# Kernel tuning notes

Hardware: AMD Instinct MI355X
Metric: run time of the kernel (lower is better)

Reference implementation:

```python
import jax, jax.numpy as jnp
import numpy as np

B, T, E, H = 2, 2048, 2048, 16
D = E // H  # head dim = 128
ROPE_BASE = 10000.0


def setup_inputs() -> dict:
    key = jax.random.key(0)
    ks = jax.random.split(key, 9)
    s = 1.0 / np.sqrt(E)
    return {
        "x": jax.random.normal(ks[0], (B, T, E), jnp.float32),
        "Wq": jax.random.normal(ks[1], (E, E), jnp.float32) * s,
        "bq": jax.random.normal(ks[2], (E,), jnp.float32) * s,
        "Wk": jax.random.normal(ks[3], (E, E), jnp.float32) * s,
        "bk": jax.random.normal(ks[4], (E,), jnp.float32) * s,
        "Wv": jax.random.normal(ks[5], (E, E), jnp.float32) * s,
        "bv": jax.random.normal(ks[6], (E,), jnp.float32) * s,
        "Wo": jax.random.normal(ks[7], (E, E), jnp.float32) * s,
        "bo": jax.random.normal(ks[8], (E,), jnp.float32) * s,
    }


def _rope(x):
    # x: [b, h, t, d]; positions are 1-indexed (m+1) as in the source
    t, d = x.shape[-2], x.shape[-1]
    j = jnp.arange(d // 2, dtype=x.dtype)
    thetas = ROPE_BASE ** (-2.0 * j / d)                  # [d/2]
    m = jnp.arange(1, t + 1, dtype=x.dtype)               # [t]
    ang = m[:, None] * thetas[None, :]                    # [t, d/2]
    C = jnp.concatenate([ang, ang], axis=-1)              # [t, d]
    x_rot = jnp.concatenate([-x[..., d // 2:], x[..., :d // 2]], axis=-1)
    return x * jnp.cos(C) + x_rot * jnp.sin(C)


def reference(x, Wq, bq, Wk, bk, Wv, bv, Wo, bo):
    b, t, e = x.shape
    # projections (nn.Linear: x @ W.T + b)
    def proj(W, bias):
        y = jnp.einsum('bte,fe->btf', x, W) + bias
        return y.reshape(b, t, H, D).transpose(0, 2, 1, 3)  # b h t d
    q = _rope(proj(Wq, bq))
    k = _rope(proj(Wk, bk))
    v = proj(Wv, bv)

    scale = jnp.sqrt(jnp.asarray(D, x.dtype))
    att = jnp.einsum('bhqd,bhkd->bhqk', q, k) / scale
    causal = jnp.tril(jnp.ones((t, t), bool))
    att = jnp.where(causal, att, -jnp.inf)
    att = jax.nn.softmax(att, axis=-1)
    y = jnp.einsum('bhqk,bhkd->bhqd', att, v)
    y = y.transpose(0, 2, 1, 3).reshape(b, t, e)
    y = jnp.einsum('bte,fe->btf', y, Wo) + bo
    return y
```

## Files before the change

kernel.cpp:

```cpp
#include <hip/hip_runtime.h>
#include <hip/hip_bf16.h>

typedef __bf16 bf16_t;
typedef __bf16 bf16x4 __attribute__((ext_vector_type(4)));
typedef __bf16 bf16x8 __attribute__((ext_vector_type(8)));
typedef float  f32x4  __attribute__((ext_vector_type(4)));

#define GLD_LDS16(gptr, lptr)                                                        \
    __builtin_amdgcn_global_load_lds((__attribute__((address_space(1))) void*)(gptr),\
                                     (__attribute__((address_space(3))) void*)(lptr),\
                                     16, 0, 0)

constexpr int Bc = 2, Tc = 2048, Ec = 2048, Hc = 16, Dc = 128;
constexpr int Mtok = Bc * Tc;

__device__ __forceinline__ bf16x8 cvt8(const float* p) {
    f32x4 a = *(const f32x4*)p;
    f32x4 b = *(const f32x4*)(p + 4);
    bf16x8 r;
    r[0] = (bf16_t)a[0]; r[1] = (bf16_t)a[1];
    r[2] = (bf16_t)a[2]; r[3] = (bf16_t)a[3];
    r[4] = (bf16_t)b[0]; r[5] = (bf16_t)b[1];
    r[6] = (bf16_t)b[2]; r[7] = (bf16_t)b[3];
    return r;
}

__global__ void convert_bf16(const float* __restrict__ src, bf16_t* __restrict__ dst) {
    size_t i = ((size_t)blockIdx.x * 256 + threadIdx.x) * 8;
    *(bf16x8*)&dst[i] = cvt8(src + i);
}

__global__ void convert_w(const float* __restrict__ Wq, const float* __restrict__ Wk,
                          const float* __restrict__ Wv, const float* __restrict__ Wo,
                          bf16_t* __restrict__ w4) {
    int blk = blockIdx.x;
    int wi  = blk >> 11;
    const float* src = (wi == 0) ? Wq : (wi == 1) ? Wk : (wi == 2) ? Wv : Wo;
    bf16_t* dst = w4 + (size_t)wi * Ec * Ec;
    size_t i = ((size_t)(blk & 2047) * 256 + threadIdx.x) * 8;
    *(bf16x8*)&dst[i] = cvt8(src + i);
}

__global__ __launch_bounds__(256) void gemm_qkv_bf(const bf16_t* __restrict__ A,
                                                   const bf16_t* __restrict__ w3,
                                                   const float* __restrict__ bq,
                                                   const float* __restrict__ bk,
                                                   const float* __restrict__ bv,
                                                   bf16_t* __restrict__ qo,
                                                   bf16_t* __restrict__ ko,
                                                   bf16_t* __restrict__ vto) {
    __shared__ __align__(16) bf16_t ldsA[128 * 32];
    __shared__ __align__(16) bf16_t ldsB[128 * 32];

    const int tid  = threadIdx.x;
    const int wave = tid >> 6;
    const int lane = tid & 63;
    const int g    = lane >> 4;
    const int n16  = lane & 15;
    const int m0   = blockIdx.x * 128;
    const int mat  = blockIdx.y >> 4;
    const int n0   = (blockIdx.y & 15) * 128;
    const int row_off = (wave >> 1) * 64;
    const int col_off = (wave & 1) * 64;
    const int K = Ec;

    const bf16_t* W   = w3 + (size_t)mat * Ec * Ec;
    const float* bias = (mat == 0) ? bq : (mat == 1) ? bk : bv;

    f32x4 acc[4][4] = {};

    const int r0 = tid >> 2;
    const int cc = tid & 3;
    const size_t a0 = (size_t)(m0 + r0) * K + cc * 8;
    const size_t a1 = (size_t)(m0 + r0 + 64) * K + cc * 8;
    const size_t b0 = (size_t)(n0 + r0) * K + cc * 8;
    const size_t b1 = (size_t)(n0 + r0 + 64) * K + cc * 8;

    for (int k0 = 0; k0 < K; k0 += 32) {
        __syncthreads();
        GLD_LDS16(A + a0 + k0, &ldsA[(wave * 64) * 8]);
        GLD_LDS16(A + a1 + k0, &ldsA[(256 + wave * 64) * 8]);
        GLD_LDS16(W + b0 + k0, &ldsB[(wave * 64) * 8]);
        GLD_LDS16(W + b1 + k0, &ldsB[(256 + wave * 64) * 8]);
        __syncthreads();

        bf16x8 af[4], bfr[4];
#pragma unroll
        for (int mt = 0; mt < 4; ++mt)
            af[mt] = *(const bf16x8*)&ldsA[(row_off + mt * 16 + n16) * 32 + g * 8];
#pragma unroll
        for (int nt = 0; nt < 4; ++nt)
            bfr[nt] = *(const bf16x8*)&ldsB[(col_off + nt * 16 + n16) * 32 + g * 8];
#pragma unroll
        for (int mt = 0; mt < 4; ++mt)
#pragma unroll
            for (int nt = 0; nt < 4; ++nt)
                acc[mt][nt] = __builtin_amdgcn_mfma_f32_16x16x32_bf16(
                    af[mt], bfr[nt], acc[mt][nt], 0, 0, 0);
    }

#pragma unroll
    for (int nt = 0; nt < 4; ++nt) {
        int n = n0 + col_off + nt * 16 + n16;
        float bn = bias[n];
        int h = n >> 7, d = n & (Dc - 1);
#pragma unroll
        for (int mt = 0; mt < 4; ++mt) {
            int mb = m0 + row_off + mt * 16 + g * 4;
            int b = mb >> 11, t = mb & (Tc - 1);
            if (mat == 2) {
                bf16x4 pk;
#pragma unroll
                for (int r = 0; r < 4; ++r) pk[r] = (bf16_t)(acc[mt][nt][r] + bn);
                *(bf16x4*)&vto[(((size_t)(b * Hc + h)) * Dc + d) * Tc + t] = pk;
            } else {
                bf16_t* outb = (mat == 0) ? qo : ko;
#pragma unroll
                for (int r = 0; r < 4; ++r)
                    outb[(((size_t)(b * Hc + h)) * Tc + (t + r)) * Dc + d] =
                        (bf16_t)(acc[mt][nt][r] + bn);
            }
        }
    }
}

__global__ __launch_bounds__(256) void gemm_out_bf(const bf16_t* __restrict__ A,
                                                   const bf16_t* __restrict__ W,
                                                   const float* __restrict__ bias,
                                                   float* __restrict__ out,
                                                   int M, int N, int K) {
    __shared__ __align__(16) bf16_t ldsA[128 * 32];
    __shared__ __align__(16) bf16_t ldsB[128 * 32];

    const int tid  = threadIdx.x;
    const int wave = tid >> 6;
    const int lane = tid & 63;
    const int g    = lane >> 4;
    const int n16  = lane & 15;
    const int m0 = blockIdx.x * 128;
    const int n0 = blockIdx.y * 128;
    const int row_off = (wave >> 1) * 64;
    const int col_off = (wave & 1) * 64;

    f32x4 acc[4][4] = {};

    const int r0 = tid >> 2;
    const int cc = tid & 3;
    const size_t a0 = (size_t)(m0 + r0) * K + cc * 8;
    const size_t a1 = (size_t)(m0 + r0 + 64) * K + cc * 8;
    const size_t b0 = (size_t)(n0 + r0) * K + cc * 8;
    const size_t b1 = (size_t)(n0 + r0 + 64) * K + cc * 8;

    for (int k0 = 0; k0 < K; k0 += 32) {
        __syncthreads();
        GLD_LDS16(A + a0 + k0, &ldsA[(wave * 64) * 8]);
        GLD_LDS16(A + a1 + k0, &ldsA[(256 + wave * 64) * 8]);
        GLD_LDS16(W + b0 + k0, &ldsB[(wave * 64) * 8]);
        GLD_LDS16(W + b1 + k0, &ldsB[(256 + wave * 64) * 8]);
        __syncthreads();

        bf16x8 af[4], bfr[4];
#pragma unroll
        for (int mt = 0; mt < 4; ++mt)
            af[mt] = *(const bf16x8*)&ldsA[(row_off + mt * 16 + n16) * 32 + g * 8];
#pragma unroll
        for (int nt = 0; nt < 4; ++nt)
            bfr[nt] = *(const bf16x8*)&ldsB[(col_off + nt * 16 + n16) * 32 + g * 8];
#pragma unroll
        for (int mt = 0; mt < 4; ++mt)
#pragma unroll
            for (int nt = 0; nt < 4; ++nt)
                acc[mt][nt] = __builtin_amdgcn_mfma_f32_16x16x32_bf16(
                    af[mt], bfr[nt], acc[mt][nt], 0, 0, 0);
    }

#pragma unroll
    for (int nt = 0; nt < 4; ++nt) {
        int n = n0 + col_off + nt * 16 + n16;
        float bn = bias[n];
#pragma unroll
        for (int mt = 0; mt < 4; ++mt) {
            int mb = m0 + row_off + mt * 16 + g * 4;
#pragma unroll
            for (int r = 0; r < 4; ++r)
                out[(size_t)(mb + r) * N + n] = acc[mt][nt][r] + bn;
        }
    }
}

__global__ __launch_bounds__(256) void gemm_qkv(const bf16_t* __restrict__ A,
                                                const float* __restrict__ Wq,
                                                const float* __restrict__ Wk,
                                                const float* __restrict__ Wv,
                                                const float* __restrict__ bq,
                                                const float* __restrict__ bk,
                                                const float* __restrict__ bv,
                                                bf16_t* __restrict__ qo,
                                                bf16_t* __restrict__ ko,
                                                bf16_t* __restrict__ vto) {
    __shared__ __align__(16) bf16_t ldsA[128 * 32];
    __shared__ __align__(16) bf16_t ldsB[128 * 32];

    const int tid  = threadIdx.x;
    const int wave = tid >> 6;
    const int lane = tid & 63;
    const int g    = lane >> 4;
    const int n16  = lane & 15;
    const int m0   = blockIdx.x * 128;
    const int mat  = blockIdx.y >> 4;
    const int n0   = (blockIdx.y & 15) * 128;
    const int row_off = (wave >> 1) * 64;
    const int col_off = (wave & 1) * 64;
    const int K = Ec;

    const float* W    = (mat == 0) ? Wq : (mat == 1) ? Wk : Wv;
    const float* bias = (mat == 0) ? bq : (mat == 1) ? bk : bv;

    f32x4 acc[4][4] = {};

    const int r0 = tid >> 2;
    const int cc = tid & 3;
    const size_t a0 = (size_t)(m0 + r0) * K + cc * 8;
    const size_t a1 = (size_t)(m0 + r0 + 64) * K + cc * 8;
    const float* pb0 = W + (size_t)(n0 + r0) * K + cc * 8;
    const float* pb1 = W + (size_t)(n0 + r0 + 64) * K + cc * 8;

    for (int k0 = 0; k0 < K; k0 += 32) {
        bf16x8 vb0 = cvt8(pb0 + k0);
        bf16x8 vb1 = cvt8(pb1 + k0);
        __syncthreads();
        GLD_LDS16(A + a0 + k0, &ldsA[(wave * 64) * 8]);
        GLD_LDS16(A + a1 + k0, &ldsA[(256 + wave * 64) * 8]);
        *(bf16x8*)&ldsB[(size_t)tid * 8]         = vb0;
        *(bf16x8*)&ldsB[(size_t)(256 + tid) * 8] = vb1;
        __syncthreads();

        bf16x8 af[4], bfr[4];
#pragma unroll
        for (int mt = 0; mt < 4; ++mt)
            af[mt] = *(const bf16x8*)&ldsA[(row_off + mt * 16 + n16) * 32 + g * 8];
#pragma unroll
        for (int nt = 0; nt < 4; ++nt)
            bfr[nt] = *(const bf16x8*)&ldsB[(col_off + nt * 16 + n16) * 32 + g * 8];
#pragma unroll
        for (int mt = 0; mt < 4; ++mt)
#pragma unroll
            for (int nt = 0; nt < 4; ++nt)
                acc[mt][nt] = __builtin_amdgcn_mfma_f32_16x16x32_bf16(
                    af[mt], bfr[nt], acc[mt][nt], 0, 0, 0);
    }

#pragma unroll
    for (int nt = 0; nt < 4; ++nt) {
        int n = n0 + col_off + nt * 16 + n16;
        float bn = bias[n];
        int h = n >> 7, d = n & (Dc - 1);
#pragma unroll
        for (int mt = 0; mt < 4; ++mt) {
            int mb = m0 + row_off + mt * 16 + g * 4;
            int b = mb >> 11, t = mb & (Tc - 1);
            if (mat == 2) {
                bf16x4 pk;
#pragma unroll
                for (int r = 0; r < 4; ++r) pk[r] = (bf16_t)(acc[mt][nt][r] + bn);
                *(bf16x4*)&vto[(((size_t)(b * Hc + h)) * Dc + d) * Tc + t] = pk;
            } else {
                bf16_t* outb = (mat == 0) ? qo : ko;
#pragma unroll
                for (int r = 0; r < 4; ++r)
                    outb[(((size_t)(b * Hc + h)) * Tc + (t + r)) * Dc + d] =
                        (bf16_t)(acc[mt][nt][r] + bn);
            }
        }
    }
}

__global__ __launch_bounds__(256) void gemm_out(const bf16_t* __restrict__ A,
                                                const float* __restrict__ W,
                                                const float* __restrict__ bias,
                                                float* __restrict__ out,
                                                int M, int N, int K) {
    __shared__ __align__(16) bf16_t ldsA[128 * 32];
    __shared__ __align__(16) bf16_t ldsB[128 * 32];

    const int tid  = threadIdx.x;
    const int wave = tid >> 6;
    const int lane = tid & 63;
    const int g    = lane >> 4;
    const int n16  = lane & 15;
    const int m0 = blockIdx.x * 128;
    const int n0 = blockIdx.y * 128;
    const int row_off = (wave >> 1) * 64;
    const int col_off = (wave & 1) * 64;

    f32x4 acc[4][4] = {};

    const int r0 = tid >> 2;
    const int cc = tid & 3;
    const size_t a0 = (size_t)(m0 + r0) * K + cc * 8;
    const size_t a1 = (size_t)(m0 + r0 + 64) * K + cc * 8;
    const float* pb0 = W + (size_t)(n0 + r0) * K + cc * 8;
    const float* pb1 = W + (size_t)(n0 + r0 + 64) * K + cc * 8;

    for (int k0 = 0; k0 < K; k0 += 32) {
        bf16x8 vb0 = cvt8(pb0 + k0);
        bf16x8 vb1 = cvt8(pb1 + k0);
        __syncthreads();
        GLD_LDS16(A + a0 + k0, &ldsA[(wave * 64) * 8]);
        GLD_LDS16(A + a1 + k0, &ldsA[(256 + wave * 64) * 8]);
        *(bf16x8*)&ldsB[(size_t)tid * 8]         = vb0;
        *(bf16x8*)&ldsB[(size_t)(256 + tid) * 8] = vb1;
        __syncthreads();

        bf16x8 af[4], bfr[4];
#pragma unroll
        for (int mt = 0; mt < 4; ++mt)
            af[mt] = *(const bf16x8*)&ldsA[(row_off + mt * 16 + n16) * 32 + g * 8];
#pragma unroll
        for (int nt = 0; nt < 4; ++nt)
            bfr[nt] = *(const bf16x8*)&ldsB[(col_off + nt * 16 + n16) * 32 + g * 8];
#pragma unroll
        for (int mt = 0; mt < 4; ++mt)
#pragma unroll
            for (int nt = 0; nt < 4; ++nt)
                acc[mt][nt] = __builtin_amdgcn_mfma_f32_16x16x32_bf16(
                    af[mt], bfr[nt], acc[mt][nt], 0, 0, 0);
    }

#pragma unroll
    for (int nt = 0; nt < 4; ++nt) {
        int n = n0 + col_off + nt * 16 + n16;
        float bn = bias[n];
#pragma unroll
        for (int mt = 0; mt < 4; ++mt) {
            int mb = m0 + row_off + mt * 16 + g * 4;
#pragma unroll
            for (int r = 0; r < 4; ++r)
                out[(size_t)(mb + r) * N + n] = acc[mt][nt][r] + bn;
        }
    }
}

__global__ void rope_kernel(bf16_t* __restrict__ q, bf16_t* __restrict__ k) {
    int row = blockIdx.x * 4 + (threadIdx.x >> 6);
    int d   = threadIdx.x & 63;
    int t   = row & (Tc - 1);
    float theta = powf(10000.0f, -(float)d * (1.0f / 64.0f));
    float ang   = (float)(t + 1) * theta;
    float sv, cv;
    sincosf(ang, &sv, &cv);
    size_t base = (size_t)row * Dc;
    float q1 = (float)q[base + d], q2 = (float)q[base + d + 64];
    q[base + d]      = (bf16_t)(q1 * cv - q2 * sv);
    q[base + d + 64] = (bf16_t)(q2 * cv + q1 * sv);
    float k1 = (float)k[base + d], k2 = (float)k[base + d + 64];
    k[base + d]      = (bf16_t)(k1 * cv - k2 * sv);
    k[base + d + 64] = (bf16_t)(k2 * cv + k1 * sv);
}

constexpr int KP = 128 + 8;
constexpr int VP = 64 + 8;
constexpr int PP = 64 + 8;

__global__ __launch_bounds__(256) void attn_kernel(const bf16_t* __restrict__ q,
                                                   const bf16_t* __restrict__ kmat,
                                                   const bf16_t* __restrict__ vt,
                                                   bf16_t* __restrict__ out) {
    __shared__ __align__(16) bf16_t k_lds[64 * KP];
    __shared__ __align__(16) bf16_t v_lds[128 * VP];
    __shared__ __align__(16) bf16_t p_lds[4 * 16 * PP];

    const int tid  = threadIdx.x;
    const int wave = tid >> 6, lane = tid & 63;
    const int g = lane >> 4, n16 = lane & 15;
    const int pi = blockIdx.x;
    const int bh = blockIdx.y;
    const size_t base = (size_t)bh * Tc * Dc;
    const int b = bh >> 4, h = bh & 15;
    const float sc2 = 0.08838834764831845f * 1.4426950408889634f;
    bf16_t* pw = &p_lds[wave * 16 * PP];

    const int kr_key = tid >> 4, kr_c = tid & 15;
    const int vr_dd  = tid >> 3, vr_c = tid & 7;

#pragma unroll 1
    for (int half = 0; half < 2; ++half) {
        const int qt = half ? pi : 31 - pi;
        const int q0 = qt * 64;

        bf16x8 qf[4];
        {
            const bf16_t* qp = q + base + (size_t)(q0 + wave * 16 + n16) * Dc + g * 8;
#pragma unroll
            for (int kk = 0; kk < 4; ++kk) qf[kk] = *(const bf16x8*)(qp + kk * 32);
        }

        float m_run[4], l_run[4];
#pragma unroll
        for (int r = 0; r < 4; ++r) { m_run[r] = -1e30f; l_run[r] = 0.0f; }
        f32x4 o_acc[8] = {};

        bf16x8 rk[4], rv[4];
#pragma unroll
        for (int i = 0; i < 4; ++i)
            rk[i] = *(const bf16x8*)&kmat[base + (size_t)(i * 16 + kr_key) * Dc + kr_c * 8];
#pragma unroll
        for (int i = 0; i < 4; ++i)
            rv[i] = *(const bf16x8*)&vt[base + (size_t)(i * 32 + vr_dd) * Tc + vr_c * 8];

#pragma unroll 1
        for (int kt = 0; kt <= qt; ++kt) {
            const int k0 = kt * 64;
            __syncthreads();
#pragma unroll
            for (int i = 0; i < 4; ++i)
                *(bf16x8*)&k_lds[(i * 16 + kr_key) * KP + kr_c * 8] = rk[i];
#pragma unroll
            for (int i = 0; i < 4; ++i)
                *(bf16x8*)&v_lds[(i * 32 + vr_dd) * VP + vr_c * 8] = rv[i];
            __syncthreads();

            if (kt < qt) {
                const int kn = k0 + 64;
#pragma unroll
                for (int i = 0; i < 4; ++i)
                    rk[i] = *(const bf16x8*)&kmat[base + (size_t)(kn + i * 16 + kr_key) * Dc + kr_c * 8];
#pragma unroll
                for (int i = 0; i < 4; ++i)
                    rv[i] = *(const bf16x8*)&vt[base + (size_t)(i * 32 + vr_dd) * Tc + kn + vr_c * 8];
            }

            f32x4 s_acc[4];
#pragma unroll
            for (int nt = 0; nt < 4; ++nt) {
                f32x4 a = {};
                int key = nt * 16 + n16;
#pragma unroll
                for (int kk = 0; kk < 4; ++kk) {
                    bf16x8 kf = *(const bf16x8*)&k_lds[key * KP + kk * 32 + g * 8];
                    a = __builtin_amdgcn_mfma_f32_16x16x32_bf16(qf[kk], kf, a, 0, 0, 0);
                }
                s_acc[nt] = a;
            }

            if (kt == qt) {
#pragma unroll
                for (int nt = 0; nt < 4; ++nt) {
                    int key = k0 + nt * 16 + n16;
#pragma unroll
                    for (int r = 0; r < 4; ++r) {
                        int qq = q0 + wave * 16 + g * 4 + r;
                        float v = s_acc[nt][r] * sc2;
                        s_acc[nt][r] = (key <= qq) ? v : -1e30f;
                    }
                }
            } else {
#pragma unroll
                for (int nt = 0; nt < 4; ++nt)
#pragma unroll
                    for (int r = 0; r < 4; ++r) s_acc[nt][r] *= sc2;
            }

            float alpha[4];
#pragma unroll
            for (int r = 0; r < 4; ++r) {
                float rm = fmaxf(fmaxf(s_acc[0][r], s_acc[1][r]),
                                 fmaxf(s_acc[2][r], s_acc[3][r]));
                rm = fmaxf(rm, __shfl_xor(rm, 1, 16));
                rm = fmaxf(rm, __shfl_xor(rm, 2, 16));
                rm = fmaxf(rm, __shfl_xor(rm, 4, 16));
                rm = fmaxf(rm, __shfl_xor(rm, 8, 16));
                float m_new = fmaxf(m_run[r], rm);
                alpha[r] = __builtin_amdgcn_exp2f(m_run[r] - m_new);
                m_run[r] = m_new;
                float sum = 0.0f;
#pragma unroll
                for (int nt = 0; nt < 4; ++nt) {
                    float p = __builtin_amdgcn_exp2f(s_acc[nt][r] - m_new);
                    s_acc[nt][r] = p;
                    sum += p;
                }
                l_run[r] = l_run[r] * alpha[r] + sum;
            }
#pragma unroll
            for (int dt = 0; dt < 8; ++dt)
#pragma unroll
                for (int r = 0; r < 4; ++r) o_acc[dt][r] *= alpha[r];

#pragma unroll
            for (int nt = 0; nt < 4; ++nt) {
                int key = nt * 16 + n16;
#pragma unroll
                for (int r = 0; r < 4; ++r)
                    pw[(g * 4 + r) * PP + key] = (bf16_t)s_acc[nt][r];
            }
            bf16x8 pf[2];
#pragma unroll
            for (int kk = 0; kk < 2; ++kk)
                pf[kk] = *(const bf16x8*)&pw[n16 * PP + kk * 32 + g * 8];

#pragma unroll
            for (int dt = 0; dt < 8; ++dt) {
                int dd = dt * 16 + n16;
#pragma unroll
                for (int kk = 0; kk < 2; ++kk) {
                    bf16x8 vf = *(const bf16x8*)&v_lds[dd * VP + kk * 32 + g * 8];
                    o_acc[dt] = __builtin_amdgcn_mfma_f32_16x16x32_bf16(
                        pf[kk], vf, o_acc[dt], 0, 0, 0);
                }
            }
        }

        float inv_l[4];
#pragma unroll
        for (int r = 0; r < 4; ++r) {
            float s = l_run[r];
            s += __shfl_xor(s, 1, 16);
            s += __shfl_xor(s, 2, 16);
            s += __shfl_xor(s, 4, 16);
            s += __shfl_xor(s, 8, 16);
            inv_l[r] = 1.0f / s;
        }
#pragma unroll
        for (int dt = 0; dt < 8; ++dt) {
            int d = dt * 16 + n16;
#pragma unroll
            for (int r = 0; r < 4; ++r) {
                int qq = q0 + wave * 16 + g * 4 + r;
                out[((size_t)(b * Tc + qq)) * Ec + h * Dc + d] =
                    (bf16_t)(o_acc[dt][r] * inv_l[r]);
            }
        }
    }
}

extern "C" void kernel_launch(void* const* d_in, const int* in_sizes, int n_in,
                              void* d_out, int out_size, void* d_ws, size_t ws_size,
                              hipStream_t stream) {
    const float* x  = (const float*)d_in[0];
    const float* Wq = (const float*)d_in[1];
    const float* bq = (const float*)d_in[2];
    const float* Wk = (const float*)d_in[3];
    const float* bk = (const float*)d_in[4];
    const float* Wv = (const float*)d_in[5];
    const float* bv = (const float*)d_in[6];
    const float* Wo = (const float*)d_in[7];
    const float* bo = (const float*)d_in[8];
    float* out = (float*)d_out;

    char* ws = (char*)d_ws;
    const size_t sz  = (size_t)Bc * Hc * Tc * Dc * sizeof(bf16_t);
    const size_t szW = (size_t)Ec * Ec * sizeof(bf16_t);
    bf16_t* q   = (bf16_t*)(ws);
    bf16_t* k   = (bf16_t*)(ws + sz);
    bf16_t* vt  = (bf16_t*)(ws + 2 * sz);
    bf16_t* xb  = (bf16_t*)(ws + 3 * sz);
    bf16_t* att = xb;

    if (ws_size >= 4 * sz + 4 * szW) {
        bf16_t* w4 = (bf16_t*)(ws + 4 * sz);
        convert_bf16<<<Mtok * Ec / (256 * 8), 256, 0, stream>>>(x, xb);
        convert_w<<<8192, 256, 0, stream>>>(Wq, Wk, Wv, Wo, w4);
        gemm_qkv_bf<<<dim3(Mtok / 128, 48), 256, 0, stream>>>(xb, w4, bq, bk, bv,
                                                              q, k, vt);
        rope_kernel<<<Bc * Hc * Tc / 4, 256, 0, stream>>>(q, k);
        attn_kernel<<<dim3(16, Bc * Hc), 256, 0, stream>>>(q, k, vt, att);
        gemm_out_bf<<<dim3(Mtok / 128, Ec / 128), 256, 0, stream>>>(
            att, w4 + 3 * (size_t)Ec * Ec, bo, out, Mtok, Ec, Ec);
    } else {
        convert_bf16<<<Mtok * Ec / (256 * 8), 256, 0, stream>>>(x, xb);
        gemm_qkv<<<dim3(Mtok / 128, 48), 256, 0, stream>>>(xb, Wq, Wk, Wv,
                                                           bq, bk, bv, q, k, vt);
        rope_kernel<<<Bc * Hc * Tc / 4, 256, 0, stream>>>(q, k);
        attn_kernel<<<dim3(16, Bc * Hc), 256, 0, stream>>>(q, k, vt, att);
        gemm_out<<<dim3(Mtok / 128, Ec / 128), 256, 0, stream>>>(att, Wo, bo, out,
                                                                 Mtok, Ec, Ec);
    }
}
```

Before: 434.1 us.

## Triple-buffer bf16 projection GEMMs with 256x128 tiles and swizzled LDS

Replaces the QKV and output projection GEMMs with 512-thread, 256x128-tile kernels that keep three LDS stages and prefetch two K-steps ahead using direct global-to-LDS loads. They wait on vmcnt instead of double __syncthreads and XOR-swizzle the LDS columns to avoid bank conflicts. MFMA sections are raised in priority. This targets the load-to-compute stalls of the single-buffered loop, at the cost of more LDS per block and hand-counted waitcnt logic that could break if the load count changes.

```diff
diff --git a/kernel.cpp b/kernel.cpp
--- a/kernel.cpp
+++ b/kernel.cpp
@@ -41,64 +41,94 @@
     *(bf16x8*)&dst[i] = cvt8(src + i);
 }
 
-__global__ __launch_bounds__(256) void gemm_qkv_bf(const bf16_t* __restrict__ A,
-                                                   const bf16_t* __restrict__ w3,
-                                                   const float* __restrict__ bq,
-                                                   const float* __restrict__ bk,
-                                                   const float* __restrict__ bv,
-                                                   bf16_t* __restrict__ qo,
-                                                   bf16_t* __restrict__ ko,
-                                                   bf16_t* __restrict__ vto) {
-    __shared__ __align__(16) bf16_t ldsA[128 * 32];
-    __shared__ __align__(16) bf16_t ldsB[128 * 32];
+
+__global__ __launch_bounds__(512, 2) void gemm_qkv_p(const bf16_t* __restrict__ A,
+                                                     const bf16_t* __restrict__ w3,
+                                                     const float* __restrict__ bq,
+                                                     const float* __restrict__ bk,
+                                                     const float* __restrict__ bv,
+                                                     bf16_t* __restrict__ qo,
+                                                     bf16_t* __restrict__ ko,
+                                                     bf16_t* __restrict__ vto) {
+    __shared__ __align__(16) bf16_t ldsA[3 * 256 * 32];
+    __shared__ __align__(16) bf16_t ldsB[3 * 128 * 32];
 
     const int tid  = threadIdx.x;
     const int wave = tid >> 6;
     const int lane = tid & 63;
     const int g    = lane >> 4;
     const int n16  = lane & 15;
-    const int m0   = blockIdx.x * 128;
+    const int wm   = wave >> 1;
+    const int wn   = wave & 1;
+    const int m0   = blockIdx.x * 256;
     const int mat  = blockIdx.y >> 4;
     const int n0   = (blockIdx.y & 15) * 128;
-    const int row_off = (wave >> 1) * 64;
-    const int col_off = (wave & 1) * 64;
-    const int K = Ec;
+    const int K    = Ec;
 
     const bf16_t* W   = w3 + (size_t)mat * Ec * Ec;
     const float* bias = (mat == 0) ? bq : (mat == 1) ? bk : bv;
 
+    const int sr   = tid >> 2;
+    const int scol = (((tid & 3) ^ ((tid >> 3) & 3)) << 3);
+    const bf16_t* gA0 = A + (size_t)(m0 + sr) * K + scol;
+    const bf16_t* gA1 = A + (size_t)(m0 + 128 + sr) * K + scol;
+    const bf16_t* gB  = W + (size_t)(n0 + sr) * K + scol;
+    const int dL = wave * 512;
+
+    const int fsw = (n16 >> 1) & 3;
+    const int rAo = (wm * 64 + n16) * 32 + ((g ^ fsw) << 3);
+    const int rBo = (wn * 64 + n16) * 32 + ((g ^ fsw) << 3);
+
     f32x4 acc[4][4] = {};
 
-    const int r0 = tid >> 2;
-    const int cc = tid & 3;
-    const size_t a0 = (size_t)(m0 + r0) * K + cc * 8;
-    const size_t a1 = (size_t)(m0 + r0 + 64) * K + cc * 8;
-    const size_t b0 = (size_t)(n0 + r0) * K + cc * 8;
-    const size_t b1 = (size_t)(n0 + r0 + 64) * K + cc * 8;
-
-    for (int k0 = 0; k0 < K; k0 += 32) {
-        __syncthreads();
-        GLD_LDS16(A + a0 + k0, &ldsA[(wave * 64) * 8]);
-        GLD_LDS16(A + a1 + k0, &ldsA[(256 + wave * 64) * 8]);
-        GLD_LDS16(W + b0 + k0, &ldsB[(wave * 64) * 8]);
-        GLD_LDS16(W + b1 + k0, &ldsB[(256 + wave * 64) * 8]);
-        __syncthreads();
-
+    constexpr int NT = Ec / 32;
+#pragma unroll
+    for (int tt = 0; tt < 2; ++tt) {
+        GLD_LDS16(gA0 + tt * 32, &ldsA[tt * 8192 + dL]);
+        GLD_LDS16(gA1 + tt * 32, &ldsA[tt * 8192 + 4096 + dL]);
+        GLD_LDS16(gB  + tt * 32, &ldsB[tt * 4096 + dL]);
+    }
+
+    int bc = 0;
+    int bi = 2;
+#pragma unroll 1
+    for (int t = 0; t < NT; ++t) {
+        if (t < NT - 1) { asm volatile("s_waitcnt vmcnt(3)" ::: "memory"); }
+        else            { asm volatile("s_waitcnt vmcnt(0)" ::: "memory"); }
+        __builtin_amdgcn_s_barrier();
+        asm volatile("" ::: "memory");
+
+        const bf16_t* la = &ldsA[bc * 8192];
+        const bf16_t* lb = &ldsB[bc * 4096];
         bf16x8 af[4], bfr[4];
 #pragma unroll
-        for (int mt = 0; mt < 4; ++mt)
-            af[mt] = *(const bf16x8*)&ldsA[(row_off + mt * 16 + n16) * 32 + g * 8];
-#pragma unroll
-        for (int nt = 0; nt < 4; ++nt)
-            bfr[nt] = *(const bf16x8*)&ldsB[(col_off + nt * 16 + n16) * 32 + g * 8];
+        for (int mt = 0; mt < 4; ++mt) af[mt] = *(const bf16x8*)&la[rAo + mt * 512];
+#pragma unroll
+        for (int nt = 0; nt < 4; ++nt) bfr[nt] = *(const bf16x8*)&lb[rBo + nt * 512];
+
+        if (t + 2 < NT) {
+            GLD_LDS16(gA0 + (t + 2) * 32, &ldsA[bi * 8192 + dL]);
+            GLD_LDS16(gA1 + (t + 2) * 32, &ldsA[bi * 8192 + 4096 + dL]);
+            GLD_LDS16(gB  + (t + 2) * 32, &ldsB[bi * 4096 + dL]);
+        }
+
+        asm volatile("s_waitcnt lgkmcnt(0)" ::: "memory");
+        __builtin_amdgcn_sched_barrier(0);
+        __builtin_amdgcn_s_setprio(1);
 #pragma unroll
         for (int mt = 0; mt < 4; ++mt)
 #pragma unroll
             for (int nt = 0; nt < 4; ++nt)
                 acc[mt][nt] = __builtin_amdgcn_mfma_f32_16x16x32_bf16(
                     af[mt], bfr[nt], acc[mt][nt], 0, 0, 0);
-    }
-
+        __builtin_amdgcn_s_setprio(0);
+
+        bc = (bc == 2) ? 0 : bc + 1;
+        bi = (bi == 2) ? 0 : bi + 1;
+    }
+
+    const int row_off = wm * 64;
+    const int col_off = wn * 64;
 #pragma unroll
     for (int nt = 0; nt < 4; ++nt) {
         int n = n0 + col_off + nt * 16 + n16;
@@ -107,73 +137,101 @@
 #pragma unroll
         for (int mt = 0; mt < 4; ++mt) {
             int mb = m0 + row_off + mt * 16 + g * 4;
-            int b = mb >> 11, t = mb & (Tc - 1);
+            int b = mb >> 11, tk = mb & (Tc - 1);
             if (mat == 2) {
                 bf16x4 pk;
 #pragma unroll
                 for (int r = 0; r < 4; ++r) pk[r] = (bf16_t)(acc[mt][nt][r] + bn);
-                *(bf16x4*)&vto[(((size_t)(b * Hc + h)) * Dc + d) * Tc + t] = pk;
+                *(bf16x4*)&vto[(((size_t)(b * Hc + h)) * Dc + d) * Tc + tk] = pk;
             } else {
                 bf16_t* outb = (mat == 0) ? qo : ko;
 #pragma unroll
                 for (int r = 0; r < 4; ++r)
-                    outb[(((size_t)(b * Hc + h)) * Tc + (t + r)) * Dc + d] =
+                    outb[(((size_t)(b * Hc + h)) * Tc + (tk + r)) * Dc + d] =
                         (bf16_t)(acc[mt][nt][r] + bn);
             }
         }
     }
 }
 
-__global__ __launch_bounds__(256) void gemm_out_bf(const bf16_t* __restrict__ A,
-                                                   const bf16_t* __restrict__ W,
-                                                   const float* __restrict__ bias,
-                                                   float* __restrict__ out,
-                                                   int M, int N, int K) {
-    __shared__ __align__(16) bf16_t ldsA[128 * 32];
-    __shared__ __align__(16) bf16_t ldsB[128 * 32];
+__global__ __launch_bounds__(512, 2) void gemm_out_p(const bf16_t* __restrict__ A,
+                                                     const bf16_t* __restrict__ W,
+                                                     const float* __restrict__ bias,
+                                                     float* __restrict__ out) {
+    __shared__ __align__(16) bf16_t ldsA[3 * 256 * 32];
+    __shared__ __align__(16) bf16_t ldsB[3 * 128 * 32];
 
     const int tid  = threadIdx.x;
     const int wave = tid >> 6;
     const int lane = tid & 63;
     const int g    = lane >> 4;
     const int n16  = lane & 15;
-    const int m0 = blockIdx.x * 128;
-    const int n0 = blockIdx.y * 128;
-    const int row_off = (wave >> 1) * 64;
-    const int col_off = (wave & 1) * 64;
+    const int wm   = wave >> 1;
+    const int wn   = wave & 1;
+    const int m0   = blockIdx.x * 256;
+    const int n0   = blockIdx.y * 128;
+    const int K    = Ec;
+
+    const int sr   = tid >> 2;
+    const int scol = (((tid & 3) ^ ((tid >> 3) & 3)) << 3);
+    const bf16_t* gA0 = A + (size_t)(m0 + sr) * K + scol;
+    const bf16_t* gA1 = A + (size_t)(m0 + 128 + sr) * K + scol;
+    const bf16_t* gB  = W + (size_t)(n0 + sr) * K + scol;
+    const int dL = wave * 512;
+
+    const int fsw = (n16 >> 1) & 3;
+    const int rAo = (wm * 64 + n16) * 32 + ((g ^ fsw) << 3);
+    const int rBo = (wn * 64 + n16) * 32 + ((g ^ fsw) << 3);
 
     f32x4 acc[4][4] = {};
 
-    const int r0 = tid >> 2;
-    const int cc = tid & 3;
-    const size_t a0 = (size_t)(m0 + r0) * K + cc * 8;
-    const size_t a1 = (size_t)(m0 + r0 + 64) * K + cc * 8;
-    const size_t b0 = (size_t)(n0 + r0) * K + cc * 8;
-    const size_t b1 = (size_t)(n0 + r0 + 64) * K + cc * 8;
-
-    for (int k0 = 0; k0 < K; k0 += 32) {
-        __syncthreads();
-        GLD_LDS16(A + a0 + k0, &ldsA[(wave * 64) * 8]);
-        GLD_LDS16(A + a1 + k0, &ldsA[(256 + wave * 64) * 8]);
-        GLD_LDS16(W + b0 + k0, &ldsB[(wave * 64) * 8]);
-        GLD_LDS16(W + b1 + k0, &ldsB[(256 + wave * 64) * 8]);
-        __syncthreads();
-
+    constexpr int NT = Ec / 32;
+#pragma unroll
+    for (int tt = 0; tt < 2; ++tt) {
+        GLD_LDS16(gA0 + tt * 32, &ldsA[tt * 8192 + dL]);
+        GLD_LDS16(gA1 + tt * 32, &ldsA[tt * 8192 + 4096 + dL]);
+        GLD_LDS16(gB  + tt * 32, &ldsB[tt * 4096 + dL]);
+    }
+
+    int bc = 0, bi = 2;
+#pragma unroll 1
+    for (int t = 0; t < NT; ++t) {
+        if (t < NT - 1) { asm volatile("s_waitcnt vmcnt(3)" ::: "memory"); }
+        else            { asm volatile("s_waitcnt vmcnt(0)" ::: "memory"); }
+        __builtin_amdgcn_s_barrier();
+        asm volatile("" ::: "memory");
+
+        const bf16_t* la = &ldsA[bc * 8192];
+        const bf16_t* lb = &ldsB[bc * 4096];
         bf16x8 af[4], bfr[4];
 #pragma unroll
-        for (int mt = 0; mt < 4; ++mt)
-            af[mt] = *(const bf16x8*)&ldsA[(row_off + mt * 16 + n16) * 32 + g * 8];
-#pragma unroll
-        for (int nt = 0; nt < 4; ++nt)
-            bfr[nt] = *(const bf16x8*)&ldsB[(col_off + nt * 16 + n16) * 32 + g * 8];
+        for (int mt = 0; mt < 4; ++mt) af[mt] = *(const bf16x8*)&la[rAo + mt * 512];
+#pragma unroll
+        for (int nt = 0; nt < 4; ++nt) bfr[nt] = *(const bf16x8*)&lb[rBo + nt * 512];
+
+        if (t + 2 < NT) {
+            GLD_LDS16(gA0 + (t + 2) * 32, &ldsA[bi * 8192 + dL]);
+            GLD_LDS16(gA1 + (t + 2) * 32, &ldsA[bi * 8192 + 4096 + dL]);
+            GLD_LDS16(gB  + (t + 2) * 32, &ldsB[bi * 4096 + dL]);
+        }
+
+        asm volatile("s_waitcnt lgkmcnt(0)" ::: "memory");
+        __builtin_amdgcn_sched_barrier(0);
+        __builtin_amdgcn_s_setprio(1);
 #pragma unroll
         for (int mt = 0; mt < 4; ++mt)
 #pragma unroll
             for (int nt = 0; nt < 4; ++nt)
                 acc[mt][nt] = __builtin_amdgcn_mfma_f32_16x16x32_bf16(
                     af[mt], bfr[nt], acc[mt][nt], 0, 0, 0);
-    }
-
+        __builtin_amdgcn_s_setprio(0);
+
+        bc = (bc == 2) ? 0 : bc + 1;
+        bi = (bi == 2) ? 0 : bi + 1;
+    }
+
+    const int row_off = wm * 64;
+    const int col_off = wn * 64;
 #pragma unroll
     for (int nt = 0; nt < 4; ++nt) {
         int n = n0 + col_off + nt * 16 + n16;
@@ -183,7 +241,7 @@
             int mb = m0 + row_off + mt * 16 + g * 4;
 #pragma unroll
             for (int r = 0; r < 4; ++r)
-                out[(size_t)(mb + r) * N + n] = acc[mt][nt][r] + bn;
+                out[(size_t)(mb + r) * Ec + n] = acc[mt][nt][r] + bn;
         }
     }
 }
@@ -561,12 +619,12 @@
         bf16_t* w4 = (bf16_t*)(ws + 4 * sz);
         convert_bf16<<<Mtok * Ec / (256 * 8), 256, 0, stream>>>(x, xb);
         convert_w<<<8192, 256, 0, stream>>>(Wq, Wk, Wv, Wo, w4);
-        gemm_qkv_bf<<<dim3(Mtok / 128, 48), 256, 0, stream>>>(xb, w4, bq, bk, bv,
-                                                              q, k, vt);
+        gemm_qkv_p<<<dim3(Mtok / 256, 48), 512, 0, stream>>>(xb, w4, bq, bk, bv,
+                                                             q, k, vt);
         rope_kernel<<<Bc * Hc * Tc / 4, 256, 0, stream>>>(q, k);
         attn_kernel<<<dim3(16, Bc * Hc), 256, 0, stream>>>(q, k, vt, att);
-        gemm_out_bf<<<dim3(Mtok / 128, Ec / 128), 256, 0, stream>>>(
-            att, w4 + 3 * (size_t)Ec * Ec, bo, out, Mtok, Ec, Ec);
+        gemm_out_p<<<dim3(Mtok / 256, Ec / 128), 512, 0, stream>>>(
+            att, w4 + 3 * (size_t)Ec * Ec, bo, out);
     } else {
         convert_bf16<<<Mtok * Ec / (256 * 8), 256, 0, stream>>>(x, xb);
         gemm_qkv<<<dim3(Mtok / 128, 48), 256, 0, stream>>>(xb, Wq, Wk, Wv,
```

Measured after the change: 405.8 us. 1.07x faster.
